# Performance work log

Hardware: AMD Instinct MI355X
Metric: run time of the kernel (lower is better)

Reference implementation:

```python
import jax, jax.numpy as jnp
import numpy as np

N, E, D, G = 50000, 600000, 128, 512  # nodes, edges, embed_dim, graphs-per-batch
LN_EPS = 1e-5


def setup_inputs() -> dict:
    key = jax.random.key(0)
    ks = jax.random.split(key, 8)
    node_hidden = jax.random.normal(ks[0], (N, D), dtype=jnp.float32)
    edge_hidden = jax.random.normal(ks[1], (E, D), dtype=jnp.float32)
    # GINEConv MLP params: Linear(D, 2D) -> ReLU -> Linear(2D, D)
    W1 = jax.random.normal(ks[2], (D, 2 * D), dtype=jnp.float32) * (1.0 / np.sqrt(D))
    b1 = jnp.zeros((2 * D,), dtype=jnp.float32)
    W2 = jax.random.normal(ks[3], (2 * D, D), dtype=jnp.float32) * (1.0 / np.sqrt(2 * D))
    b2 = jnp.zeros((D,), dtype=jnp.float32)
    ln_gamma = jnp.ones((D,), dtype=jnp.float32)
    ln_beta = jnp.zeros((D,), dtype=jnp.float32)
    edge_index = jax.random.randint(ks[4], (2, E), 0, N, dtype=jnp.int32)
    node_id = jnp.sort(jax.random.randint(ks[5], (N,), 0, G, dtype=jnp.int32))
    edge_id = jnp.sort(jax.random.randint(ks[6], (E,), 0, G, dtype=jnp.int32))
    return {
        "node_hidden": node_hidden, "edge_hidden": edge_hidden,
        "W1": W1, "b1": b1, "W2": W2, "b2": b2,
        "ln_gamma": ln_gamma, "ln_beta": ln_beta,
        "edge_index": edge_index, "node_id": node_id, "edge_id": edge_id,
    }


def reference(node_hidden, edge_hidden, W1, b1, W2, b2, ln_gamma, ln_beta,
              edge_index, node_id, edge_id):
    n = node_hidden.shape[0]
    src, dst = edge_index[0], edge_index[1]
    # --- GINEConv: msg = relu(x_src + e), scatter-add at dst, (1+eps)*x + agg, MLP ---
    msg = jax.nn.relu(node_hidden[src] + edge_hidden)          # [E, D]
    agg = jax.ops.segment_sum(msg, dst, num_segments=n)        # [N, D]
    h = node_hidden + agg                                      # eps = 0 (PyG default)
    h = jax.nn.relu(jnp.dot(h, W1) + b1)
    h = jnp.dot(h, W2) + b2                                    # [N, D]
    # --- LayerNorm over feature dim ---
    mu = jnp.mean(h, axis=-1, keepdims=True)
    var = jnp.mean(jnp.square(h - mu), axis=-1, keepdims=True)
    h = (h - mu) * jax.lax.rsqrt(var + LN_EPS) * ln_gamma + ln_beta
    # --- GraphNorm: divide each node's features by sqrt(#nodes in its graph) ---
    counts = jax.ops.segment_sum(jnp.ones((n,), dtype=h.dtype), node_id,
                                 num_segments=G)               # [G]
    scale = jax.lax.rsqrt(jnp.maximum(counts, 1.0))            # [G]
    h = h * scale[node_id][:, None]
    # --- last_act=True -> ReLU; dropout is identity in eval; residual add ---
    h = jax.nn.relu(h)
    return h + node_hidden
```

## Files before the change

kernel.cpp:

```cpp
#include <hip/hip_runtime.h>
#include <hip/hip_bf16.h>

#define N_NODES 50000
#define N_EDGES 600000
#define DIM     128
#define HID     256
#define NGRAPH  512
#define LN_EPS  1e-5f
#define CAP     40
#define OVFCAP  4096

typedef __attribute__((ext_vector_type(8))) short bf16x8;
typedef __attribute__((ext_vector_type(4))) float f32x4;

__device__ __forceinline__ unsigned short f2bf(float x) {
  unsigned int u = __builtin_bit_cast(unsigned int, x);
  unsigned int r = (u + 0x7FFFu + ((u >> 16) & 1u)) >> 16;
  return (unsigned short)r;
}

__global__ void k_init(int* __restrict__ deg, int* __restrict__ counts,
                       int* __restrict__ ovf_cnt) {
  int i = blockIdx.x * 256 + threadIdx.x;
  if (i < N_NODES) deg[i] = 0;
  if (i < NGRAPH) counts[i] = 0;
  if (i == 0) *ovf_cnt = 0;
}

__global__ void k_prep_weights(const float* __restrict__ W1, const float* __restrict__ W2,
                               unsigned char* __restrict__ blob) {
  int id = blockIdx.x * 256 + threadIdx.x;
  union { unsigned short s[8]; uint4 v; } u;
  if (id < 4096) {
    int c  = id >> 4;
    int k0 = (id & 15) * 8;
#pragma unroll
    for (int j = 0; j < 8; ++j) u.s[j] = f2bf(W1[(size_t)(k0 + j) * HID + c]);
    unsigned char* dst = blob + c * 256 + ((k0 * 2) ^ ((c & 7) << 4));
    *(uint4*)dst = u.v;
  } else if (id < 8192) {
    int id2 = id - 4096;
    int c  = id2 >> 5;
    int k0 = (id2 & 31) * 8;
#pragma unroll
    for (int j = 0; j < 8; ++j) u.s[j] = f2bf(W2[(size_t)(k0 + j) * DIM + c]);
    unsigned char* dst = blob + 65536 + c * 512 + ((k0 * 2) ^ ((c & 7) << 4));
    *(uint4*)dst = u.v;
  }
}

__global__ void k_scatter(const int* __restrict__ ei, const int* __restrict__ node_id,
                          int* __restrict__ deg, int* __restrict__ slots,
                          int* __restrict__ counts, int* __restrict__ ovf_cnt,
                          int* __restrict__ ovf_list) {
  int t = blockIdx.x * 256 + threadIdx.x;
  if (t < N_NODES) atomicAdd(&counts[node_id[t]], 1);
  if (t < N_EDGES) {
    int dst = ei[N_EDGES + t];
    int pos = atomicAdd(&deg[dst], 1);
    if (pos < CAP) {
      slots[(size_t)dst * CAP + pos] = t;
    } else {
      int o = atomicAdd(ovf_cnt, 1);
      if (o < OVFCAP) ovf_list[o] = t;
    }
  }
}

__global__ __launch_bounds__(256) void k_gather(
    const float2* __restrict__ nh2, const float2* __restrict__ eh2,
    const int* __restrict__ ei, const int* __restrict__ deg,
    const int* __restrict__ slots, float2* __restrict__ out2) {
  int node = blockIdx.x * 4 + (threadIdx.x >> 6);
  int lane = threadIdx.x & 63;
  if (node >= N_NODES) return;
  int d = deg[node];
  if (d > CAP) d = CAP;
  int e = 0, s = 0;
  if (lane < d) {
    e = slots[(size_t)node * CAP + lane];
    s = ei[e];
  }
  float2 acc = make_float2(0.f, 0.f);
  for (int i = 0; i < d; ++i) {
    int ee = __shfl(e, i);
    int ss = __shfl(s, i);
    float2 x = nh2[(size_t)ss * 64 + lane];
    float2 y = eh2[(size_t)ee * 64 + lane];
    acc.x += fmaxf(x.x + y.x, 0.f);
    acc.y += fmaxf(x.y + y.y, 0.f);
  }
  out2[(size_t)node * 64 + lane] = acc;
}

__global__ void k_ovf(const int* __restrict__ ovf_list, const int* __restrict__ ovf_cnt,
                      const float4* __restrict__ nh4, const float4* __restrict__ eh4,
                      const int* __restrict__ ei, float* __restrict__ acc) {
  int cnt = *ovf_cnt;
  if (cnt > OVFCAP) cnt = OVFCAP;
  int t = blockIdx.x * 256 + threadIdx.x;
  int q = t & 31;
  for (int idx = t >> 5; idx < cnt; idx += (16 * 256) >> 5) {
    int e = ovf_list[idx];
    int src = ei[e];
    int dst = ei[N_EDGES + e];
    float4 a = nh4[(size_t)src * 32 + q];
    float4 b = eh4[(size_t)e * 32 + q];
    float m0 = fmaxf(a.x + b.x, 0.f);
    float m1 = fmaxf(a.y + b.y, 0.f);
    float m2 = fmaxf(a.z + b.z, 0.f);
    float m3 = fmaxf(a.w + b.w, 0.f);
    float* p = acc + (size_t)dst * DIM + q * 4;
    if (m0 > 0.f) atomicAdd(p + 0, m0);
    if (m1 > 0.f) atomicAdd(p + 1, m1);
    if (m2 > 0.f) atomicAdd(p + 2, m2);
    if (m3 > 0.f) atomicAdd(p + 3, m3);
  }
}

__global__ __launch_bounds__(512, 2) void k_mlp(
    const float* acc, const float* __restrict__ nh,
    const unsigned char* __restrict__ blob,
    const float* __restrict__ b1v, const float* __restrict__ b2v,
    const float* __restrict__ gam, const float* __restrict__ bet,
    const int* __restrict__ node_id, const int* __restrict__ counts,
    float* outp) {
  __shared__ unsigned char lds[131072];
  const int tid  = threadIdx.x;
  const int lane = tid & 63;
  const int wave = tid >> 6;
  const int l15  = lane & 15;
  const int lhi  = lane >> 4;
  const int swz  = (lane & 7) << 4;

  {
    const uint4* s = (const uint4*)blob;
    uint4* d = (uint4*)lds;
#pragma unroll
    for (int i = 0; i < 16; ++i) d[tid + i * 512] = s[tid + i * 512];
  }
  __syncthreads();

  const int row0 = blockIdx.x * 128 + wave * 16;
  const int arow = row0 + l15;
  const bool aok = arow < N_NODES;
  const float* ap = acc + (size_t)arow * DIM + lhi * 8;
  const float* np = nh + (size_t)arow * DIM + lhi * 8;

  f32x4 c1[16];
#pragma unroll
  for (int i = 0; i < 16; ++i) c1[i] = (f32x4){0.f, 0.f, 0.f, 0.f};

#pragma unroll
  for (int ks = 0; ks < 4; ++ks) {
    bf16x8 af;
    if (aok) {
      float4 x0 = *(const float4*)(ap + ks * 32);
      float4 x1 = *(const float4*)(ap + ks * 32 + 4);
      float4 y0 = *(const float4*)(np + ks * 32);
      float4 y1 = *(const float4*)(np + ks * 32 + 4);
      af[0] = (short)f2bf(x0.x + y0.x);
      af[1] = (short)f2bf(x0.y + y0.y);
      af[2] = (short)f2bf(x0.z + y0.z);
      af[3] = (short)f2bf(x0.w + y0.w);
      af[4] = (short)f2bf(x1.x + y1.x);
      af[5] = (short)f2bf(x1.y + y1.y);
      af[6] = (short)f2bf(x1.z + y1.z);
      af[7] = (short)f2bf(x1.w + y1.w);
    } else {
#pragma unroll
      for (int j = 0; j < 8; ++j) af[j] = 0;
    }
#pragma unroll
    for (int ct = 0; ct < 16; ++ct) {
      int c = ct * 16 + l15;
      const bf16x8* bp = (const bf16x8*)(lds + c * 256 + ((ks * 64 + lhi * 16) ^ swz));
      c1[ct] = __builtin_amdgcn_mfma_f32_16x16x32_bf16(af, *bp, c1[ct], 0, 0, 0);
    }
  }
  __syncthreads();

  unsigned char* hb = lds + wave * 8192;
#pragma unroll
  for (int ct = 0; ct < 16; ++ct) {
    int c = ct * 16 + l15;
    float bb = b1v[c];
#pragma unroll
    for (int i = 0; i < 4; ++i) {
      int r = lhi * 4 + i;
      float v = fmaxf(c1[ct][i] + bb, 0.f);
      *(unsigned short*)(hb + r * 512 + ((2 * c) ^ ((r & 7) << 4))) = f2bf(v);
    }
  }
  __syncthreads();

  f32x4 c2[8];
#pragma unroll
  for (int i = 0; i < 8; ++i) c2[i] = (f32x4){0.f, 0.f, 0.f, 0.f};

#pragma unroll
  for (int ks = 0; ks < 8; ++ks) {
    bf16x8 af = *(const bf16x8*)(hb + l15 * 512 + ((ks * 64 + lhi * 16) ^ swz));
#pragma unroll
    for (int ct = 0; ct < 8; ++ct) {
      int c = ct * 16 + l15;
      const bf16x8* bp = (const bf16x8*)(lds + 65536 + c * 512 + ((ks * 64 + lhi * 16) ^ swz));
      c2[ct] = __builtin_amdgcn_mfma_f32_16x16x32_bf16(af, *bp, c2[ct], 0, 0, 0);
    }
  }

  float vbuf[8][4];
  float s[4] = {0.f, 0.f, 0.f, 0.f}, sq[4] = {0.f, 0.f, 0.f, 0.f};
#pragma unroll
  for (int ct = 0; ct < 8; ++ct) {
    float bb = b2v[ct * 16 + l15];
#pragma unroll
    for (int i = 0; i < 4; ++i) {
      float x = c2[ct][i] + bb;
      vbuf[ct][i] = x;
      s[i] += x;
      sq[i] += x * x;
    }
  }
#pragma unroll
  for (int m = 1; m <= 8; m <<= 1) {
#pragma unroll
    for (int i = 0; i < 4; ++i) {
      s[i] += __shfl_xor(s[i], m, 64);
      sq[i] += __shfl_xor(sq[i], m, 64);
    }
  }
  float mu[4], rstd[4], gs[4];
  int rr[4];
  bool rok[4];
#pragma unroll
  for (int i = 0; i < 4; ++i) {
    mu[i] = s[i] * (1.f / 128.f);
    float var = sq[i] * (1.f / 128.f) - mu[i] * mu[i];
    rstd[i] = rsqrtf(var + LN_EPS);
    rr[i] = row0 + lhi * 4 + i;
    rok[i] = rr[i] < N_NODES;
    int g = rok[i] ? node_id[rr[i]] : 0;
    gs[i] = rsqrtf(fmaxf((float)counts[g], 1.f));
  }
#pragma unroll
  for (int ct = 0; ct < 8; ++ct) {
    int c = ct * 16 + l15;
    float gg = gam[c], be = bet[c];
#pragma unroll
    for (int i = 0; i < 4; ++i) {
      if (rok[i]) {
        float y = (vbuf[ct][i] - mu[i]) * rstd[i] * gg + be;
        y *= gs[i];
        y = fmaxf(y, 0.f);
        y += nh[(size_t)rr[i] * DIM + c];
        outp[(size_t)rr[i] * DIM + c] = y;
      }
    }
  }
}

extern "C" void kernel_launch(void* const* d_in, const int* in_sizes, int n_in,
                              void* d_out, int out_size, void* d_ws, size_t ws_size,
                              hipStream_t stream) {
  const float* node_hidden = (const float*)d_in[0];
  const float* edge_hidden = (const float*)d_in[1];
  const float* W1  = (const float*)d_in[2];
  const float* b1  = (const float*)d_in[3];
  const float* W2  = (const float*)d_in[4];
  const float* b2  = (const float*)d_in[5];
  const float* lng = (const float*)d_in[6];
  const float* lnb = (const float*)d_in[7];
  const int* edge_index = (const int*)d_in[8];
  const int* node_id    = (const int*)d_in[9];
  float* out = (float*)d_out;

  unsigned char* ws = (unsigned char*)d_ws;
  unsigned char* blob = ws;
  int* counts   = (int*)(ws + 131072);
  int* ovf_cnt  = (int*)(ws + 133120);
  int* ovf_list = (int*)(ws + 133184);
  int* deg      = (int*)(ws + 163840);
  int* slots    = (int*)(ws + 393216);

  k_init<<<196, 256, 0, stream>>>(deg, counts, ovf_cnt);
  k_prep_weights<<<32, 256, 0, stream>>>(W1, W2, blob);
  k_scatter<<<2344, 256, 0, stream>>>(edge_index, node_id, deg, slots,
                                      counts, ovf_cnt, ovf_list);
  k_gather<<<12500, 256, 0, stream>>>((const float2*)node_hidden,
                                      (const float2*)edge_hidden,
                                      edge_index, deg, slots, (float2*)out);
  k_ovf<<<16, 256, 0, stream>>>(ovf_list, ovf_cnt, (const float4*)node_hidden,
                                (const float4*)edge_hidden, edge_index, out);
  k_mlp<<<391, 512, 0, stream>>>(out, node_hidden, blob, b1, b2, lng, lnb,
                                 node_id, counts, out);
}
```

Before: 215.5 us.

## Pack edge/src pairs in slots, gather two nodes per wave with float4 loads

The scatter kernel now stores (edge, src) pairs, so the gather no longer does a dependent load of edge_index. Each wave now handles two nodes with 32 lanes each, using 16-byte loads and nontemporal loads for edge features. The self term node_hidden is folded into the gather accumulator, so the MLP no longer reloads it. The init and weight-prep kernels are merged into one launch. In exchange, the slots buffer doubles in size, and lanes idle when the two nodes in a wave have very different degrees.

Result: faster. 207.3 us (-3.8%).

```diff
diff --git a/kernel.cpp b/kernel.cpp
--- a/kernel.cpp
+++ b/kernel.cpp
@@ -19,17 +19,14 @@
   return (unsigned short)r;
 }
 
-__global__ void k_init(int* __restrict__ deg, int* __restrict__ counts,
-                       int* __restrict__ ovf_cnt) {
-  int i = blockIdx.x * 256 + threadIdx.x;
-  if (i < N_NODES) deg[i] = 0;
-  if (i < NGRAPH) counts[i] = 0;
-  if (i == 0) *ovf_cnt = 0;
-}
-
-__global__ void k_prep_weights(const float* __restrict__ W1, const float* __restrict__ W2,
-                               unsigned char* __restrict__ blob) {
+__global__ void k_init_prep(const float* __restrict__ W1, const float* __restrict__ W2,
+                            unsigned char* __restrict__ blob,
+                            int* __restrict__ deg, int* __restrict__ counts,
+                            int* __restrict__ ovf_cnt) {
   int id = blockIdx.x * 256 + threadIdx.x;
+  if (id < N_NODES) deg[id] = 0;
+  if (id < NGRAPH) counts[id] = 0;
+  if (id == 0) *ovf_cnt = 0;
   union { unsigned short s[8]; uint4 v; } u;
   if (id < 4096) {
     int c  = id >> 4;
@@ -50,16 +47,17 @@
 }
 
 __global__ void k_scatter(const int* __restrict__ ei, const int* __restrict__ node_id,
-                          int* __restrict__ deg, int* __restrict__ slots,
+                          int* __restrict__ deg, int2* __restrict__ slots2,
                           int* __restrict__ counts, int* __restrict__ ovf_cnt,
                           int* __restrict__ ovf_list) {
   int t = blockIdx.x * 256 + threadIdx.x;
   if (t < N_NODES) atomicAdd(&counts[node_id[t]], 1);
   if (t < N_EDGES) {
+    int src = ei[t];
     int dst = ei[N_EDGES + t];
     int pos = atomicAdd(&deg[dst], 1);
     if (pos < CAP) {
-      slots[(size_t)dst * CAP + pos] = t;
+      slots2[(size_t)dst * CAP + pos] = make_int2(t, src);
     } else {
       int o = atomicAdd(ovf_cnt, 1);
       if (o < OVFCAP) ovf_list[o] = t;
@@ -68,29 +66,42 @@
 }
 
 __global__ __launch_bounds__(256) void k_gather(
-    const float2* __restrict__ nh2, const float2* __restrict__ eh2,
-    const int* __restrict__ ei, const int* __restrict__ deg,
-    const int* __restrict__ slots, float2* __restrict__ out2) {
-  int node = blockIdx.x * 4 + (threadIdx.x >> 6);
+    const f32x4* __restrict__ nh4, const f32x4* __restrict__ eh4,
+    const int* __restrict__ deg, const int2* __restrict__ slots2,
+    f32x4* __restrict__ out4) {
+  int w    = blockIdx.x * 4 + (threadIdx.x >> 6);
   int lane = threadIdx.x & 63;
-  if (node >= N_NODES) return;
+  int l31  = lane & 31;
+  int base = lane & 32;
+  int node = w * 2 + (lane >> 5);
   int d = deg[node];
   if (d > CAP) d = CAP;
-  int e = 0, s = 0;
-  if (lane < d) {
-    e = slots[(size_t)node * CAP + lane];
-    s = ei[e];
-  }
-  float2 acc = make_float2(0.f, 0.f);
-  for (int i = 0; i < d; ++i) {
-    int ee = __shfl(e, i);
-    int ss = __shfl(s, i);
-    float2 x = nh2[(size_t)ss * 64 + lane];
-    float2 y = eh2[(size_t)ee * 64 + lane];
-    acc.x += fmaxf(x.x + y.x, 0.f);
-    acc.y += fmaxf(x.y + y.y, 0.f);
-  }
-  out2[(size_t)node * 64 + lane] = acc;
+  int2 s0 = make_int2(0, 0), s1 = make_int2(0, 0);
+  const int2* sp = slots2 + (size_t)node * CAP;
+  if (l31 < d) s0 = sp[l31];
+  if (l31 < 8 && 32 + l31 < d) s1 = sp[32 + l31];
+  int dmax = max(d, __shfl(d, lane ^ 32));
+  f32x4 acc = nh4[(size_t)node * 32 + l31];
+#pragma unroll 2
+  for (int i = 0; i < dmax; ++i) {
+    int ee, ss;
+    if (i < 32) {
+      ee = __shfl(s0.x, base + i);
+      ss = __shfl(s0.y, base + i);
+    } else {
+      ee = __shfl(s1.x, base + (i - 32));
+      ss = __shfl(s1.y, base + (i - 32));
+    }
+    if (i < d) {
+      f32x4 x = nh4[(size_t)ss * 32 + l31];
+      f32x4 y = __builtin_nontemporal_load(&eh4[(size_t)ee * 32 + l31]);
+      acc.x += fmaxf(x.x + y.x, 0.f);
+      acc.y += fmaxf(x.y + y.y, 0.f);
+      acc.z += fmaxf(x.z + y.z, 0.f);
+      acc.w += fmaxf(x.w + y.w, 0.f);
+    }
+  }
+  out4[(size_t)node * 32 + l31] = acc;
 }
 
 __global__ void k_ovf(const int* __restrict__ ovf_list, const int* __restrict__ ovf_cnt,
@@ -145,7 +156,6 @@
   const int arow = row0 + l15;
   const bool aok = arow < N_NODES;
   const float* ap = acc + (size_t)arow * DIM + lhi * 8;
-  const float* np = nh + (size_t)arow * DIM + lhi * 8;
 
   f32x4 c1[16];
 #pragma unroll
@@ -157,16 +167,14 @@
     if (aok) {
       float4 x0 = *(const float4*)(ap + ks * 32);
       float4 x1 = *(const float4*)(ap + ks * 32 + 4);
-      float4 y0 = *(const float4*)(np + ks * 32);
-      float4 y1 = *(const float4*)(np + ks * 32 + 4);
-      af[0] = (short)f2bf(x0.x + y0.x);
-      af[1] = (short)f2bf(x0.y + y0.y);
-      af[2] = (short)f2bf(x0.z + y0.z);
-      af[3] = (short)f2bf(x0.w + y0.w);
-      af[4] = (short)f2bf(x1.x + y1.x);
-      af[5] = (short)f2bf(x1.y + y1.y);
-      af[6] = (short)f2bf(x1.z + y1.z);
-      af[7] = (short)f2bf(x1.w + y1.w);
+      af[0] = (short)f2bf(x0.x);
+      af[1] = (short)f2bf(x0.y);
+      af[2] = (short)f2bf(x0.z);
+      af[3] = (short)f2bf(x0.w);
+      af[4] = (short)f2bf(x1.x);
+      af[5] = (short)f2bf(x1.y);
+      af[6] = (short)f2bf(x1.z);
+      af[7] = (short)f2bf(x1.w);
     } else {
 #pragma unroll
       for (int j = 0; j < 8; ++j) af[j] = 0;
@@ -281,15 +289,14 @@
   int* ovf_cnt  = (int*)(ws + 133120);
   int* ovf_list = (int*)(ws + 133184);
   int* deg      = (int*)(ws + 163840);
-  int* slots    = (int*)(ws + 393216);
-
-  k_init<<<196, 256, 0, stream>>>(deg, counts, ovf_cnt);
-  k_prep_weights<<<32, 256, 0, stream>>>(W1, W2, blob);
-  k_scatter<<<2344, 256, 0, stream>>>(edge_index, node_id, deg, slots,
+  int2* slots2  = (int2*)(ws + 393216);
+
+  k_init_prep<<<196, 256, 0, stream>>>(W1, W2, blob, deg, counts, ovf_cnt);
+  k_scatter<<<2344, 256, 0, stream>>>(edge_index, node_id, deg, slots2,
                                       counts, ovf_cnt, ovf_list);
-  k_gather<<<12500, 256, 0, stream>>>((const float2*)node_hidden,
-                                      (const float2*)edge_hidden,
-                                      edge_index, deg, slots, (float2*)out);
+  k_gather<<<6250, 256, 0, stream>>>((const f32x4*)node_hidden,
+                                     (const f32x4*)edge_hidden,
+                                     deg, slots2, (f32x4*)out);
   k_ovf<<<16, 256, 0, stream>>>(ovf_list, ovf_cnt, (const float4*)node_hidden,
                                 (const float4*)edge_hidden, edge_index, out);
   k_mlp<<<391, 512, 0, stream>>>(out, node_hidden, blob, b1, b2, lng, lnb,
```
